# Optimization experiments

Hardware: AMD Instinct MI355X
Metric: run time of the kernel (lower is better)

## Reference

```python
import jax, jax.numpy as jnp
import numpy as np
from functools import partial

VOCAB = 32000
N_LAYER = 2
D_MODEL = 1024
D_INNER = 2048   # expand * d_model
D_STATE = 16
D_CONV = 4
DT_RANK = 64     # ceil(d_model/16)
SEQ_LEN = 2048   # == D_INNER (required by the repo's conv quirk)
BATCH = 1
EPS = 1e-6


def rmsnorm(x, scale):
    return x * jax.lax.rsqrt(jnp.mean(x * x, axis=-1, keepdims=True) + EPS) * scale


def setup_inputs() -> dict:
    key = jax.random.key(0)
    ks = jax.random.split(key, 16)
    s = 0.02
    L = N_LAYER
    inp = {
        "input_ids": jax.random.randint(ks[0], (BATCH, SEQ_LEN), 0, VOCAB, dtype=jnp.int32),
        "embed": jax.random.normal(ks[1], (VOCAB, D_MODEL), jnp.float32) * s,
        "norm_scale": jnp.ones((L, D_MODEL), jnp.float32),
        "in_proj_w": jax.random.normal(ks[2], (L, D_MODEL, 2 * D_INNER), jnp.float32) * s,
        "in_proj_b": jnp.zeros((L, 2 * D_INNER), jnp.float32),
        "conv_w": jax.random.normal(ks[3], (L, D_CONV, 1, SEQ_LEN), jnp.float32) * s,
        "conv_b": jnp.zeros((L, SEQ_LEN), jnp.float32),
        "x_proj_w": jax.random.normal(ks[4], (L, D_MODEL, DT_RANK + 2 * D_STATE), jnp.float32) * s,
        "dt_proj_w": jax.random.normal(ks[5], (L, DT_RANK, D_INNER), jnp.float32) * s,
        "dt_proj_b": jnp.zeros((L, D_INNER), jnp.float32),
        "out_proj_w": jax.random.normal(ks[6], (L, D_INNER, D_MODEL), jnp.float32) * s,
        "out_proj_b": jnp.zeros((L, D_MODEL), jnp.float32),
        "A_log": jnp.tile(jnp.log(jnp.arange(1, D_STATE + 1, dtype=jnp.float32)), (L, D_INNER, 1)),
        "D_param": jnp.ones((L, D_INNER), jnp.float32),
        "norm_f_scale": jnp.ones((D_MODEL,), jnp.float32),
        "lm_head_w": jax.random.normal(ks[7], (D_MODEL, VOCAB), jnp.float32) * s,
    }
    return inp


def selective_scan(u, delta, A, B, C, D):
    # u, delta: (b,l,d)   A: (d,n)   B,C: (b,l,n)   D: (d,)
    deltaA = jnp.exp(jnp.einsum('bld,dn->bldn', delta, A))            # (b,l,d,n)
    deltaB_u = delta[..., None] * B[:, :, None, :] * u[..., None]      # (b,l,d,n)

    def step(x, inps):
        dA, dBu, c = inps            # (b,d,n),(b,d,n),(b,n)
        x = dA * x + dBu
        y = jnp.einsum('bdn,bn->bd', x, c)
        return x, y

    x0 = jnp.zeros((u.shape[0], u.shape[2], A.shape[1]), u.dtype)
    _, ys = jax.lax.scan(step, x0, (jnp.moveaxis(deltaA, 1, 0),
                                    jnp.moveaxis(deltaB_u, 1, 0),
                                    jnp.moveaxis(C, 1, 0)))
    return jnp.moveaxis(ys, 0, 1) + u * D                              # (b,l,d)


def depthwise_conv(x, w, b):
    # Faithful to repo: Conv(features=SEQ_LEN, groups=D_INNER) on (b, d_inner, l).
    # With SEQ_LEN == D_INNER this is a depthwise conv over the d_inner axis.
    # x: (b, d_inner, l) as (N, W, C);  w: (d_conv, 1, SEQ_LEN)
    y = jax.lax.conv_general_dilated(x, w, window_strides=(1,), padding='SAME',
                                     dimension_numbers=('NWC', 'WIO', 'NWC'),
                                     feature_group_count=SEQ_LEN)
    return y + b


def mamba_block(h, norm_scale, in_w, in_b, conv_w, conv_b, x_proj_w,
                dt_w, dt_b, out_w, out_b, A_log, Dp):
    u = rmsnorm(h, norm_scale)
    A = -jnp.exp(A_log)
    x_and_res = u @ in_w + in_b
    x, res = jnp.split(x_and_res, 2, axis=-1)
    xt = jnp.transpose(x, (0, 2, 1))                 # (b, d_inner, l)
    xt = depthwise_conv(xt, conv_w, conv_b)[:, :, :u.shape[1]]
    x = jax.nn.silu(jnp.transpose(xt, (0, 2, 1)))     # (b, l, d_inner)
    x_dbl = u @ x_proj_w
    delta, B, C = jnp.split(x_dbl, [DT_RANK, DT_RANK + D_STATE], axis=-1)
    delta = jax.nn.softplus(delta @ dt_w + dt_b)
    y = selective_scan(x, delta, A, B, C, Dp)
    y = y * jax.nn.silu(res)
    return y @ out_w + out_b + h


def reference(input_ids, embed, norm_scale, in_proj_w, in_proj_b, conv_w, conv_b,
              x_proj_w, dt_proj_w, dt_proj_b, out_proj_w, out_proj_b, A_log,
              D_param, norm_f_scale, lm_head_w):
    h = embed[input_ids]                              # (b,l,d_model)
    for i in range(N_LAYER):
        h = mamba_block(h, norm_scale[i], in_proj_w[i], in_proj_b[i], conv_w[i],
                        conv_b[i], x_proj_w[i], dt_proj_w[i], dt_proj_b[i],
                        out_proj_w[i], out_proj_b[i], A_log[i], D_param[i])
    h = rmsnorm(h, norm_f_scale)
    return h @ lm_head_w                              # (b,l,vocab)
```

## Files before the change

### kernel.cpp

```cpp
#include <hip/hip_runtime.h>
#include <hip/hip_bf16.h>

#define SEQ 2048
#define DM  1024
#define DI  2048
#define DST 16
#define DTR 64
#define NVOC 32000
#define NVOCP 32768
#define NC  64
#define LC  32

typedef __bf16 bf16x8 __attribute__((ext_vector_type(8)));
typedef float  f32x4  __attribute__((ext_vector_type(4)));

__device__ __forceinline__ float siluf(float x) { return x / (1.f + expf(-x)); }
__device__ __forceinline__ float softplusf(float x) {
    return fmaxf(x, 0.f) + log1pf(expf(-fabsf(x)));
}
__device__ __forceinline__ unsigned short f2bf(float f) {
    union { __hip_bfloat16 h; unsigned short u; } c;
    c.h = __float2bfloat16(f);
    return c.u;
}

__global__ void embed_gather(const int* __restrict__ ids, const float* __restrict__ embed,
                             float* __restrict__ h) {
    int l = blockIdx.x;
    int row = ids[l];
    const float4* src = (const float4*)(embed + (size_t)row * DM);
    float4* dst = (float4*)(h + (size_t)l * DM);
    dst[threadIdx.x] = src[threadIdx.x];
}

__global__ void rmsnorm_kernel(const float* __restrict__ x, const float* __restrict__ w,
                               float* __restrict__ o, unsigned short* __restrict__ ob) {
    int l = blockIdx.x;
    int t = threadIdx.x;
    float4 v = ((const float4*)(x + (size_t)l * DM))[t];
    float ss = v.x*v.x + v.y*v.y + v.z*v.z + v.w*v.w;
    #pragma unroll
    for (int m = 32; m; m >>= 1) ss += __shfl_xor(ss, m);
    __shared__ float red[4];
    if ((t & 63) == 0) red[t >> 6] = ss;
    __syncthreads();
    float tot = red[0] + red[1] + red[2] + red[3];
    float sc = rsqrtf(tot * (1.f / DM) + 1e-6f);
    float4 wv = ((const float4*)w)[t];
    float4 ov;
    ov.x = v.x * sc * wv.x;
    ov.y = v.y * sc * wv.y;
    ov.z = v.z * sc * wv.z;
    ov.w = v.w * sc * wv.w;
    if (ob) {
        uint2 pk;
        pk.x = (unsigned)f2bf(ov.x) | ((unsigned)f2bf(ov.y) << 16);
        pk.y = (unsigned)f2bf(ov.z) | ((unsigned)f2bf(ov.w) << 16);
        ((uint2*)(ob + (size_t)l * DM))[t] = pk;
    } else {
        ((float4*)(o + (size_t)l * DM))[t] = ov;
    }
}

__global__ void transpose_all(const float* __restrict__ in_w, const float* __restrict__ xp_w,
                              const float* __restrict__ out_w, const float* __restrict__ dt_w,
                              const float* __restrict__ lm_w,
                              unsigned short* __restrict__ in_wT, unsigned short* __restrict__ out_wT,
                              unsigned short* __restrict__ dt_wT, unsigned short* __restrict__ lm_wT) {
    int b = blockIdx.x;
    const float* W; unsigned short* WT; int K, N, Np, loc;
    if      (b < 1024)  { W = in_w;                        WT = in_wT;                                             K=1024; N=4096;  Np=4096;  loc = b; }
    else if (b < 1056)  { W = xp_w;                        WT = in_wT + (size_t)4096 * 1024;                       K=1024; N=96;    Np=128;   loc = b - 1024; }
    else if (b < 2080)  { W = in_w + (size_t)1024 * 4096;  WT = in_wT + (size_t)4224 * 1024;                       K=1024; N=4096;  Np=4096;  loc = b - 1056; }
    else if (b < 2112)  { W = xp_w + (size_t)1024 * 96;    WT = in_wT + (size_t)4224 * 1024 + (size_t)4096 * 1024; K=1024; N=96;    Np=128;   loc = b - 2080; }
    else if (b < 2624)  { W = out_w;                       WT = out_wT;                                            K=2048; N=1024;  Np=1024;  loc = b - 2112; }
    else if (b < 3136)  { W = out_w + (size_t)2048 * 1024; WT = out_wT + (size_t)1024 * 2048;                      K=2048; N=1024;  Np=1024;  loc = b - 2624; }
    else if (b < 3168)  { W = dt_w;                        WT = dt_wT;                                             K=64;   N=2048;  Np=2048;  loc = b - 3136; }
    else if (b < 3200)  { W = dt_w + (size_t)64 * 2048;    WT = dt_wT + (size_t)2048 * 64;                         K=64;   N=2048;  Np=2048;  loc = b - 3168; }
    else                { if (!lm_wT) return; W = lm_w;    WT = lm_wT;                                             K=1024; N=32000; Np=32768; loc = b - 3200; }
    int tiles_x = Np >> 6;
    int n0 = (loc % tiles_x) * 64, k0 = (loc / tiles_x) * 64;
    __shared__ float tile[64][65];
    int tx = threadIdx.x;
    int ty = threadIdx.y;
    #pragma unroll
    for (int i = 0; i < 8; i++) {
        int r = ty + i * 8;
        int n1 = n0 + tx, n2 = n0 + tx + 32;
        tile[tx][r]      = (n1 < N) ? W[(size_t)(k0 + r) * N + n1] : 0.f;
        tile[tx + 32][r] = (n2 < N) ? W[(size_t)(k0 + r) * N + n2] : 0.f;
    }
    __syncthreads();
    int t = ty * 32 + tx;
    int nrow = t >> 5;
    int u = t & 31;
    #pragma unroll
    for (int pass = 0; pass < 8; pass++) {
        int n = pass * 8 + nrow;
        unsigned v = (unsigned)f2bf(tile[n][2 * u]) | ((unsigned)f2bf(tile[n][2 * u + 1]) << 16);
        *(unsigned*)&WT[(size_t)(n0 + n) * K + k0 + 2 * u] = v;
    }
}

template<int ACT>
__global__ __launch_bounds__(256) void gemm_f32(const float* __restrict__ A, int lda,
                                                const float* __restrict__ B,
                                                const float* __restrict__ bias,
                                                const float* __restrict__ add,
                                                float* __restrict__ C,
                                                int M, int N, int K) {
    __shared__ float As[16][68];
    __shared__ float Bs[16][64];
    int tx = threadIdx.x, ty = threadIdx.y;
    int t = ty * 16 + tx;
    int m0 = blockIdx.y * 64, n0 = blockIdx.x * 64;
    float acc[4][4] = {};
    for (int k0 = 0; k0 < K; k0 += 16) {
        #pragma unroll
        for (int i = 0; i < 4; i++) {
            int idx = t + i * 256;
            int mm = idx >> 4, kk = idx & 15;
            As[kk][mm] = A[(size_t)(m0 + mm) * lda + k0 + kk];
            int nn = idx & 63, k2 = idx >> 6;
            Bs[k2][nn] = B[(size_t)(k0 + k2) * N + n0 + nn];
        }
        __syncthreads();
        #pragma unroll
        for (int kk = 0; kk < 16; kk++) {
            float4 a = *(const float4*)&As[kk][ty * 4];
            float4 b = *(const float4*)&Bs[kk][tx * 4];
            acc[0][0] += a.x*b.x; acc[0][1] += a.x*b.y; acc[0][2] += a.x*b.z; acc[0][3] += a.x*b.w;
            acc[1][0] += a.y*b.x; acc[1][1] += a.y*b.y; acc[1][2] += a.y*b.z; acc[1][3] += a.y*b.w;
            acc[2][0] += a.z*b.x; acc[2][1] += a.z*b.y; acc[2][2] += a.z*b.z; acc[2][3] += a.z*b.w;
            acc[3][0] += a.w*b.x; acc[3][1] += a.w*b.y; acc[3][2] += a.w*b.z; acc[3][3] += a.w*b.w;
        }
        __syncthreads();
    }
    #pragma unroll
    for (int i = 0; i < 4; i++) {
        int row = m0 + ty * 4 + i;
        float4 r;
        float* pr = &r.x;
        #pragma unroll
        for (int j = 0; j < 4; j++) {
            int col = n0 + tx * 4 + j;
            float v = acc[i][j];
            if (bias) v += bias[col];
            if (add)  v += add[(size_t)row * N + col];
            if (ACT == 1) v = softplusf(v);
            pr[j] = v;
        }
        *(float4*)&C[(size_t)row * N + n0 + tx * 4] = r;
    }
}

template<int BIAS, int ADD, int ACT, int XP>
__global__ __launch_bounds__(256) void gemm_bf16(const unsigned short* __restrict__ A, int lda,
                                                 const unsigned short* __restrict__ BT,
                                                 const float* __restrict__ bias,
                                                 const float* __restrict__ add,
                                                 float* __restrict__ C,
                                                 float* __restrict__ xp_out,
                                                 unsigned short* __restrict__ aux,
                                                 int M, int N, int K) {
    __shared__ unsigned short As[128 * 32];
    __shared__ unsigned short Bs[128 * 32];
    int t = threadIdx.x;
    int w = t >> 6, l = t & 63;
    int wm = w >> 1, wn = w & 1;
    int m0 = blockIdx.x * 128;
    int n0 = blockIdx.y * 128;
    int lr = l & 15, lk = (l >> 4) * 8;
    int sr = t >> 2, sc = (t & 3) * 8;
    f32x4 acc[4][4] = {};
    for (int k0 = 0; k0 < K; k0 += 32) {
        const unsigned short* ga = A  + (size_t)(m0 + sr) * lda + k0 + sc;
        const unsigned short* gb = BT + (size_t)(n0 + sr) * K + k0 + sc;
        unsigned short* la = As + w * 512;
        unsigned short* lb = Bs + w * 512;
        __builtin_amdgcn_global_load_lds((const __attribute__((address_space(1))) void*)ga,
            (__attribute__((address_space(3))) void*)la, 16, 0, 0);
        __builtin_amdgcn_global_load_lds((const __attribute__((address_space(1))) void*)(ga + (size_t)64 * lda),
            (__attribute__((address_space(3))) void*)(la + 2048), 16, 0, 0);
        __builtin_amdgcn_global_load_lds((const __attribute__((address_space(1))) void*)gb,
            (__attribute__((address_space(3))) void*)(lb), 16, 0, 0);
        __builtin_amdgcn_global_load_lds((const __attribute__((address_space(1))) void*)(gb + (size_t)64 * K),
            (__attribute__((address_space(3))) void*)(lb + 2048), 16, 0, 0);
        __syncthreads();
        bf16x8 af[4], bfr[4];
        #pragma unroll
        for (int i = 0; i < 4; i++) {
            af[i]  = *reinterpret_cast<const bf16x8*>(&As[(wm * 64 + i * 16 + lr) * 32 + lk]);
            bfr[i] = *reinterpret_cast<const bf16x8*>(&Bs[(wn * 64 + i * 16 + lr) * 32 + lk]);
        }
        #pragma unroll
        for (int i = 0; i < 4; i++)
            #pragma unroll
            for (int j = 0; j < 4; j++)
                acc[i][j] = __builtin_amdgcn_mfma_f32_16x16x32_bf16(af[i], bfr[j], acc[i][j], 0, 0, 0);
        __syncthreads();
    }
    int cr = (l >> 4) * 4;
    if (XP && n0 >= 4096) {
        #pragma unroll
        for (int i = 0; i < 4; i++) {
            #pragma unroll
            for (int j = 0; j < 4; j++) {
                int c2 = (n0 - 4096) + wn * 64 + j * 16 + lr;
                #pragma unroll
                for (int rr = 0; rr < 4; rr++) {
                    int row = m0 + wm * 64 + i * 16 + cr + rr;
                    float v = acc[i][j][rr];
                    xp_out[(size_t)row * 128 + c2] = v;
                    if (c2 < 64) aux[(size_t)row * 64 + c2] = f2bf(v);
                }
            }
        }
    } else {
        int ldc = XP ? 4096 : N;
        #pragma unroll
        for (int i = 0; i < 4; i++) {
            #pragma unroll
            for (int j = 0; j < 4; j++) {
                int col = n0 + wn * 64 + j * 16 + lr;
                float bv = BIAS ? bias[col] : 0.f;
                #pragma unroll
                for (int rr = 0; rr < 4; rr++) {
                    int row = m0 + wm * 64 + i * 16 + cr + rr;
                    float v = acc[i][j][rr] + bv;
                    if (ADD) v += add[(size_t)row * ldc + col];
                    if (ACT == 1) v = softplusf(v);
                    C[(size_t)row * ldc + col] = v;
                }
            }
        }
    }
}

__global__ __launch_bounds__(1024, 4) void gemm_lm(
        const unsigned short* __restrict__ A,
        const unsigned short* __restrict__ BT,
        float* __restrict__ C, int M, int N, int K) {
    extern __shared__ unsigned short lds[];
    const int t = threadIdx.x;
    const int w = t >> 6, l = t & 63;
    const int wr = w >> 2, wc = w & 3;
    int bxx = blockIdx.x, byy = blockIdx.y;
    if (gridDim.x == 8 && (gridDim.y & 7) == 0) {
        int lin = blockIdx.y * 8 + blockIdx.x;
        int xcd = lin & 7, i = lin >> 3;
        bxx = i & 7;
        byy = xcd * (gridDim.y >> 3) + (i >> 3);
    }
    const int m0 = bxx * 256, n0 = byy * 256;
    const int lr = l & 15;
    const int rowA = wr * 64 + lr;
    const int rowB = wc * 64 + lr;
    const int colR = (((l >> 4) ^ (lr & 3)) * 8);
    const int srow = t >> 2;
    const int scol = (((t & 3) ^ (srow & 3)) * 8);
    const int NT = K >> 5;
    f32x4 acc[4][4] = {};
    bf16x8 af[4], bf[4];

    const unsigned short* gA = A  + (size_t)(m0 + srow) * K + scol;
    const unsigned short* gB = BT + (size_t)(n0 + srow) * K + scol;

    #pragma unroll
    for (int pp = 0; pp < 2; pp++) {
        if (pp < NT) {
            unsigned short* Ld = lds + pp * 16384;
            __builtin_amdgcn_global_load_lds(
                (const __attribute__((address_space(1))) void*)(gA + pp * 32),
                (__attribute__((address_space(3))) void*)(Ld + w * 512), 16, 0, 0);
            __builtin_amdgcn_global_load_lds(
                (const __attribute__((address_space(1))) void*)(gB + pp * 32),
                (__attribute__((address_space(3))) void*)(Ld + 8192 + w * 512), 16, 0, 0);
        }
    }

    for (int kt = 0; kt < NT; kt++) {
        if (kt >= NT - 2) { asm volatile("s_waitcnt vmcnt(0)" ::: "memory"); }
        else              { asm volatile("s_waitcnt vmcnt(2)" ::: "memory"); }
        __builtin_amdgcn_sched_barrier(0);
        __builtin_amdgcn_s_barrier();
        __builtin_amdgcn_sched_barrier(0);
        const unsigned short* Ab = lds + (kt % 3) * 16384;
        const unsigned short* Bb = Ab + 8192;
        #pragma unroll
        for (int i = 0; i < 4; i++)
            af[i] = *reinterpret_cast<const bf16x8*>(&Ab[(rowA + i * 16) * 32 + colR]);
        #pragma unroll
        for (int j = 0; j < 4; j++)
            bf[j] = *reinterpret_cast<const bf16x8*>(&Bb[(rowB + j * 16) * 32 + colR]);
        if (kt + 2 < NT) {
            unsigned short* Ld = lds + ((kt + 2) % 3) * 16384;
            __builtin_amdgcn_global_load_lds(
                (const __attribute__((address_space(1))) void*)(gA + (kt + 2) * 32),
                (__attribute__((address_space(3))) void*)(Ld + w * 512), 16, 0, 0);
            __builtin_amdgcn_global_load_lds(
                (const __attribute__((address_space(1))) void*)(gB + (kt + 2) * 32),
                (__attribute__((address_space(3))) void*)(Ld + 8192 + w * 512), 16, 0, 0);
        }
        __builtin_amdgcn_s_setprio(1);
        #pragma unroll
        for (int i = 0; i < 4; i++)
            #pragma unroll
            for (int j = 0; j < 4; j++)
                acc[i][j] = __builtin_amdgcn_mfma_f32_16x16x32_bf16(af[i], bf[j], acc[i][j], 0, 0, 0);
        __builtin_amdgcn_s_setprio(0);
    }

    float* cf = (float*)lds;
    const int cr = (l >> 4) * 4;
    for (int r = 0; r < 4; r++) {
        __syncthreads();
        if (wr == r) {
            #pragma unroll
            for (int i = 0; i < 4; i++)
                #pragma unroll
                for (int j = 0; j < 4; j++) {
                    int col = wc * 64 + j * 16 + lr;
                    #pragma unroll
                    for (int rr = 0; rr < 4; rr++)
                        cf[(i * 16 + cr + rr) * 260 + col] = acc[i][j][rr];
                }
        }
        __syncthreads();
        #pragma unroll
        for (int pass = 0; pass < 4; pass++) {
            int row = pass * 16 + (t >> 6);
            int f4 = t & 63;
            float4 v = *(const float4*)&cf[row * 260 + f4 * 4];
            int grow = m0 + r * 64 + row;
            int gcol = n0 + f4 * 4;
            if (gcol < N) *(float4*)&C[(size_t)grow * N + gcol] = v;
        }
    }
}

__global__ void xproj_kernel(const float* __restrict__ u, const float* __restrict__ xw,
                             float* __restrict__ xdbl) {
    int l0 = blockIdx.x * 4;
    int t = threadIdx.x;
    __shared__ float us[4][DM];
    for (int i = t; i < 4 * DM; i += 128) us[i >> 10][i & 1023] = u[(size_t)l0 * DM + i];
    __syncthreads();
    if (t < 96) {
        float a0 = 0.f, a1 = 0.f, a2 = 0.f, a3 = 0.f;
        for (int k = 0; k < DM; k++) {
            float wv = xw[(size_t)k * 96 + t];
            a0 += us[0][k] * wv; a1 += us[1][k] * wv;
            a2 += us[2][k] * wv; a3 += us[3][k] * wv;
        }
        xdbl[(size_t)(l0 + 0) * 128 + t] = a0;
        xdbl[(size_t)(l0 + 1) * 128 + t] = a1;
        xdbl[(size_t)(l0 + 2) * 128 + t] = a2;
        xdbl[(size_t)(l0 + 3) * 128 + t] = a3;
    }
}

__global__ __launch_bounds__(256) void scan_p1(const float* __restrict__ xr,
        const float* __restrict__ delta, const float* __restrict__ xdbl,
        const float* __restrict__ cw, const float* __restrict__ cb,
        const float* __restrict__ A_log, float* __restrict__ P, float* __restrict__ S) {
    int c = blockIdx.x;
    int d = blockIdx.y * 256 + threadIdx.x;
    int l0 = c * LC;
    __shared__ float Bsh[LC][16];
    __shared__ float cwsh[4][LC];
    __shared__ float cbsh[LC];
    {
        int t = threadIdx.x;
        #pragma unroll
        for (int i = t; i < LC * 16; i += 256) {
            int ll = i >> 4, q = i & 15;
            Bsh[ll][q] = xdbl[(size_t)(l0 + ll) * 128 + 64 + q];
        }
        if (t < LC) {
            cbsh[t] = cb[l0 + t];
            #pragma unroll
            for (int k = 0; k < 4; k++) cwsh[k][t] = cw[k * SEQ + l0 + t];
        }
    }
    __syncthreads();
    float a[16];
    #pragma unroll
    for (int i = 0; i < 4; i++) {
        float4 al = ((const float4*)(A_log + (size_t)d * 16))[i];
        a[4*i+0] = -expf(al.x); a[4*i+1] = -expf(al.y);
        a[4*i+2] = -expf(al.z); a[4*i+3] = -expf(al.w);
    }
    float s[16] = {};
    float sumdv = 0.f;
    for (int ll = 0; ll < LC; ll++) {
        size_t lrow = (size_t)(l0 + ll);
        float dv = delta[lrow * DI + d];
        const float* xrow = xr + lrow * 4096;
        float accv = cbsh[ll];
        #pragma unroll
        for (int k = 0; k < 4; k++) {
            int cc = d + k - 1;
            if (cc >= 0 && cc < DI) accv += xrow[cc] * cwsh[k][ll];
        }
        float xv = siluf(accv);
        float du = dv * xv;
        sumdv += dv;
        #pragma unroll
        for (int n = 0; n < 16; n++)
            s[n] = expf(dv * a[n]) * s[n] + du * Bsh[ll][n];
    }
    size_t o = ((size_t)c * DI + d) * 16;
    #pragma unroll
    for (int i = 0; i < 4; i++) {
        float4 sv = make_float4(s[4*i], s[4*i+1], s[4*i+2], s[4*i+3]);
        float4 pv = make_float4(expf(a[4*i]*sumdv), expf(a[4*i+1]*sumdv),
                                expf(a[4*i+2]*sumdv), expf(a[4*i+3]*sumdv));
        ((float4*)(S + o))[i] = sv;
        ((float4*)(P + o))[i] = pv;
    }
}

__global__ void scan_p2(const float* __restrict__ P, const float* __restrict__ S,
                        float* __restrict__ X) {
    int t = blockIdx.x * 256 + threadIdx.x;
    float x = 0.f;
    #pragma unroll 16
    for (int c = 0; c < NC; c++) {
        X[(size_t)c * (DI*16) + t] = x;
        x = P[(size_t)c * (DI*16) + t] * x + S[(size_t)c * (DI*16) + t];
    }
}

__global__ __launch_bounds__(256) void scan_p3(const float* __restrict__ xr,
        const float* __restrict__ delta, const float* __restrict__ xdbl,
        const float* __restrict__ cw, const float* __restrict__ cb,
        const float* __restrict__ A_log, const float* __restrict__ Dp,
        const float* __restrict__ X,
        float* __restrict__ y, unsigned short* __restrict__ yb) {
    int c = blockIdx.x;
    int d = blockIdx.y * 256 + threadIdx.x;
    int l0 = c * LC;
    __shared__ float Bsh[LC][16], Csh[LC][16];
    __shared__ float cwsh[4][LC];
    __shared__ float cbsh[LC];
    {
        int t = threadIdx.x;
        #pragma unroll
        for (int i = t; i < LC * 16; i += 256) {
            int ll = i >> 4, q = i & 15;
            size_t row = (size_t)(l0 + ll) * 128;
            Bsh[ll][q] = xdbl[row + 64 + q];
            Csh[ll][q] = xdbl[row + 80 + q];
        }
        if (t < LC) {
            cbsh[t] = cb[l0 + t];
            #pragma unroll
            for (int k = 0; k < 4; k++) cwsh[k][t] = cw[k * SEQ + l0 + t];
        }
    }
    __syncthreads();
    float a[16];
    #pragma unroll
    for (int i = 0; i < 4; i++) {
        float4 al = ((const float4*)(A_log + (size_t)d * 16))[i];
        a[4*i+0] = -expf(al.x); a[4*i+1] = -expf(al.y);
        a[4*i+2] = -expf(al.z); a[4*i+3] = -expf(al.w);
    }
    float s[16];
    size_t o = ((size_t)c * DI + d) * 16;
    #pragma unroll
    for (int i = 0; i < 4; i++) {
        float4 xv4 = ((const float4*)(X + o))[i];
        s[4*i] = xv4.x; s[4*i+1] = xv4.y; s[4*i+2] = xv4.z; s[4*i+3] = xv4.w;
    }
    float Dv = Dp[d];
    for (int ll = 0; ll < LC; ll++) {
        size_t lrow = (size_t)(l0 + ll);
        float dv = delta[lrow * DI + d];
        const float* xrow = xr + lrow * 4096;
        float accv = cbsh[ll];
        #pragma unroll
        for (int k = 0; k < 4; k++) {
            int cc = d + k - 1;
            if (cc >= 0 && cc < DI) accv += xrow[cc] * cwsh[k][ll];
        }
        float xv = siluf(accv);
        float du = dv * xv;
        float yv = 0.f;
        #pragma unroll
        for (int n = 0; n < 16; n++) {
            s[n] = expf(dv * a[n]) * s[n] + du * Bsh[ll][n];
            yv += s[n] * Csh[ll][n];
        }
        float res = xrow[2048 + d];
        float val = (yv + xv * Dv) * siluf(res);
        if (yb) yb[lrow * DI + d] = f2bf(val);
        else    y[lrow * DI + d] = val;
    }
}

extern "C" void kernel_launch(void* const* d_in, const int* in_sizes, int n_in,
                              void* d_out, int out_size, void* d_ws, size_t ws_size,
                              hipStream_t stream) {
    const int*   ids        = (const int*)d_in[0];
    const float* embed      = (const float*)d_in[1];
    const float* norm_scale = (const float*)d_in[2];
    const float* in_w       = (const float*)d_in[3];
    const float* in_b       = (const float*)d_in[4];
    const float* conv_w     = (const float*)d_in[5];
    const float* conv_b     = (const float*)d_in[6];
    const float* x_proj_w   = (const float*)d_in[7];
    const float* dt_w       = (const float*)d_in[8];
    const float* dt_b       = (const float*)d_in[9];
    const float* out_w      = (const float*)d_in[10];
    const float* out_b      = (const float*)d_in[11];
    const float* A_log      = (const float*)d_in[12];
    const float* Dp         = (const float*)d_in[13];
    const float* norm_f     = (const float*)d_in[14];
    const float* lm_w       = (const float*)d_in[15];

    float* out = (float*)d_out;

    char* p = (char*)d_ws;
    float* h  = (float*)p;  p += (size_t)SEQ * DM * 4;
    float* hn = (float*)p;  p += (size_t)SEQ * DM * 4;
    size_t base = (size_t)p - (size_t)d_ws;
    const size_t SZ_UB    = (size_t)SEQ * DM * 2;
    const size_t SZ_YB    = (size_t)SEQ * DI * 2;
    const size_t SZ_HNB   = (size_t)SEQ * DM * 2;
    const size_t SZ_DB    = (size_t)SEQ * 64 * 2;
    const size_t SZ_INWT  = (size_t)2 * 4224 * DM * 2;
    const size_t SZ_OUTWT = (size_t)2 * DM * DI * 2;
    const size_t SZ_DTWT  = (size_t)2 * DI * 64 * 2;
    const size_t SZ_LMWT  = (size_t)NVOCP * DM * 2;
    size_t need_mid  = base + SZ_UB + SZ_YB + SZ_HNB + SZ_DB + SZ_INWT + SZ_OUTWT + SZ_DTWT;
    size_t need_full = need_mid + SZ_LMWT;
    bool mid  = ws_size >= need_mid;
    bool full = ws_size >= need_full;

    unsigned short *u_b = nullptr, *y_b = nullptr, *hn_b = nullptr, *dlt_b = nullptr;
    unsigned short *in_wT = nullptr, *out_wT = nullptr, *dt_wT = nullptr, *lm_wT = nullptr;
    if (mid) {
        u_b    = (unsigned short*)p; p += SZ_UB;
        y_b    = (unsigned short*)p; p += SZ_YB;
        hn_b   = (unsigned short*)p; p += SZ_HNB;
        dlt_b  = (unsigned short*)p; p += SZ_DB;
        in_wT  = (unsigned short*)p; p += SZ_INWT;
        out_wT = (unsigned short*)p; p += SZ_OUTWT;
        dt_wT  = (unsigned short*)p; p += SZ_DTWT;
        if (full) { lm_wT = (unsigned short*)p; p += SZ_LMWT; }
    }

    float* u     = out;
    float* xr    = u + (size_t)SEQ * DM;
    float* xdbl  = xr + (size_t)SEQ * 4096;
    float* delta = xdbl + (size_t)SEQ * 128;
    float* y     = delta + (size_t)SEQ * DI;
    float* Pbuf  = y + (size_t)SEQ * DI;
    float* Sbuf  = Pbuf + (size_t)NC * DI * 16;
    float* Xbuf  = Sbuf + (size_t)NC * DI * 16;

    if (mid) {
        int nblocks = full ? 11392 : 3200;
        transpose_all<<<nblocks, dim3(32, 8), 0, stream>>>(
            in_w, x_proj_w, out_w, dt_w, lm_w, in_wT, out_wT, dt_wT, lm_wT);
    }

    embed_gather<<<SEQ, 256, 0, stream>>>(ids, embed, h);

    for (int L = 0; L < 2; L++) {
        rmsnorm_kernel<<<SEQ, 256, 0, stream>>>(h, norm_scale + (size_t)L * DM, u, u_b);
        if (mid) {
            gemm_bf16<1, 0, 0, 1><<<dim3(SEQ / 128, 4224 / 128), 256, 0, stream>>>(
                u_b, DM, in_wT + (size_t)L * 4224 * DM, in_b + (size_t)L * 4096, nullptr, xr,
                xdbl, dlt_b, SEQ, 4224, DM);
            gemm_bf16<1, 0, 1, 0><<<dim3(SEQ / 128, DI / 128), 256, 0, stream>>>(
                dlt_b, 64, dt_wT + (size_t)L * DI * 64, dt_b + (size_t)L * DI, nullptr, delta,
                nullptr, nullptr, SEQ, DI, 64);
        } else {
            gemm_f32<0><<<dim3(4096 / 64, SEQ / 64), dim3(16, 16), 0, stream>>>(
                u, DM, in_w + (size_t)L * DM * 4096, in_b + (size_t)L * 4096, nullptr, xr,
                SEQ, 4096, DM);
            xproj_kernel<<<SEQ / 4, 128, 0, stream>>>(u, x_proj_w + (size_t)L * DM * 96, xdbl);
            gemm_f32<1><<<dim3(DI / 64, SEQ / 64), dim3(16, 16), 0, stream>>>(
                xdbl, 128, dt_w + (size_t)L * DTR * DI, dt_b + (size_t)L * DI, nullptr, delta,
                SEQ, DI, DTR);
        }
        scan_p1<<<dim3(NC, DI / 256), 256, 0, stream>>>(
            xr, delta, xdbl, conv_w + (size_t)L * 4 * SEQ, conv_b + (size_t)L * SEQ,
            A_log + (size_t)L * DI * DST, Pbuf, Sbuf);
        scan_p2<<<DI * 16 / 256, 256, 0, stream>>>(Pbuf, Sbuf, Xbuf);
        scan_p3<<<dim3(NC, DI / 256), 256, 0, stream>>>(
            xr, delta, xdbl, conv_w + (size_t)L * 4 * SEQ, conv_b + (size_t)L * SEQ,
            A_log + (size_t)L * DI * DST, Dp + (size_t)L * DI, Xbuf, y, y_b);
        if (mid) {
            gemm_bf16<1, 1, 0, 0><<<dim3(SEQ / 128, DM / 128), 256, 0, stream>>>(
                y_b, DI, out_wT + (size_t)L * DM * DI, out_b + (size_t)L * DM, h, h,
                nullptr, nullptr, SEQ, DM, DI);
        } else {
            gemm_f32<0><<<dim3(DM / 64, SEQ / 64), dim3(16, 16), 0, stream>>>(
                y, DI, out_w + (size_t)L * DI * DM, out_b + (size_t)L * DM, h, h,
                SEQ, DM, DI);
        }
    }

    rmsnorm_kernel<<<SEQ, 256, 0, stream>>>(h, norm_f, hn, full ? hn_b : nullptr);
    if (full) {
        hipFuncSetAttribute((const void*)gemm_lm,
                            hipFuncAttributeMaxDynamicSharedMemorySize, 98304);
        gemm_lm<<<dim3(SEQ / 256, NVOCP / 256), 1024, 98304, stream>>>(
            hn_b, lm_wT, out, SEQ, NVOC, DM);
    } else {
        gemm_f32<0><<<dim3(NVOC / 64, SEQ / 64), dim3(16, 16), 0, stream>>>(
            hn, DM, lm_w, nullptr, nullptr, out, SEQ, NVOC, DM);
    }
}
```

Measured before the change: 807.2 us.

## Fuse three-phase chunked scan into one cooperative kernel with grid syncs

Replaces the three separate scan launches (chunk-local scan, cross-chunk prefix, chunk re-scan) with a single cooperative kernel that uses grid.sync between phases, keeping shared-memory staging and A coefficients live across phases. This removes two kernel launches and their drain gaps per layer. The grid is 512 blocks of 256 threads, which must all be co-resident for the cooperative launch. During the middle phase only 128 blocks work while the rest wait. The lm_head GEMM output store is also switched to a nontemporal store to avoid polluting the cache with the large logits write.

```diff
diff --git a/kernel.cpp b/kernel.cpp
--- a/kernel.cpp
+++ b/kernel.cpp
@@ -1,5 +1,8 @@
 #include <hip/hip_runtime.h>
 #include <hip/hip_bf16.h>
+#include <hip/hip_cooperative_groups.h>
+
+namespace cg = cooperative_groups;
 
 #define SEQ 2048
 #define DM  1024
@@ -331,10 +334,11 @@
         for (int pass = 0; pass < 4; pass++) {
             int row = pass * 16 + (t >> 6);
             int f4 = t & 63;
-            float4 v = *(const float4*)&cf[row * 260 + f4 * 4];
+            f32x4 v = *(const f32x4*)&cf[row * 260 + f4 * 4];
             int grow = m0 + r * 64 + row;
             int gcol = n0 + f4 * 4;
-            if (gcol < N) *(float4*)&C[(size_t)grow * N + gcol] = v;
+            if (gcol < N)
+                __builtin_nontemporal_store(v, (f32x4*)&C[(size_t)grow * N + gcol]);
         }
     }
 }
@@ -360,84 +364,14 @@
     }
 }
 
-__global__ __launch_bounds__(256) void scan_p1(const float* __restrict__ xr,
-        const float* __restrict__ delta, const float* __restrict__ xdbl,
-        const float* __restrict__ cw, const float* __restrict__ cb,
-        const float* __restrict__ A_log, float* __restrict__ P, float* __restrict__ S) {
-    int c = blockIdx.x;
-    int d = blockIdx.y * 256 + threadIdx.x;
-    int l0 = c * LC;
-    __shared__ float Bsh[LC][16];
-    __shared__ float cwsh[4][LC];
-    __shared__ float cbsh[LC];
-    {
-        int t = threadIdx.x;
-        #pragma unroll
-        for (int i = t; i < LC * 16; i += 256) {
-            int ll = i >> 4, q = i & 15;
-            Bsh[ll][q] = xdbl[(size_t)(l0 + ll) * 128 + 64 + q];
-        }
-        if (t < LC) {
-            cbsh[t] = cb[l0 + t];
-            #pragma unroll
-            for (int k = 0; k < 4; k++) cwsh[k][t] = cw[k * SEQ + l0 + t];
-        }
-    }
-    __syncthreads();
-    float a[16];
-    #pragma unroll
-    for (int i = 0; i < 4; i++) {
-        float4 al = ((const float4*)(A_log + (size_t)d * 16))[i];
-        a[4*i+0] = -expf(al.x); a[4*i+1] = -expf(al.y);
-        a[4*i+2] = -expf(al.z); a[4*i+3] = -expf(al.w);
-    }
-    float s[16] = {};
-    float sumdv = 0.f;
-    for (int ll = 0; ll < LC; ll++) {
-        size_t lrow = (size_t)(l0 + ll);
-        float dv = delta[lrow * DI + d];
-        const float* xrow = xr + lrow * 4096;
-        float accv = cbsh[ll];
-        #pragma unroll
-        for (int k = 0; k < 4; k++) {
-            int cc = d + k - 1;
-            if (cc >= 0 && cc < DI) accv += xrow[cc] * cwsh[k][ll];
-        }
-        float xv = siluf(accv);
-        float du = dv * xv;
-        sumdv += dv;
-        #pragma unroll
-        for (int n = 0; n < 16; n++)
-            s[n] = expf(dv * a[n]) * s[n] + du * Bsh[ll][n];
-    }
-    size_t o = ((size_t)c * DI + d) * 16;
-    #pragma unroll
-    for (int i = 0; i < 4; i++) {
-        float4 sv = make_float4(s[4*i], s[4*i+1], s[4*i+2], s[4*i+3]);
-        float4 pv = make_float4(expf(a[4*i]*sumdv), expf(a[4*i+1]*sumdv),
-                                expf(a[4*i+2]*sumdv), expf(a[4*i+3]*sumdv));
-        ((float4*)(S + o))[i] = sv;
-        ((float4*)(P + o))[i] = pv;
-    }
-}
-
-__global__ void scan_p2(const float* __restrict__ P, const float* __restrict__ S,
-                        float* __restrict__ X) {
-    int t = blockIdx.x * 256 + threadIdx.x;
-    float x = 0.f;
-    #pragma unroll 16
-    for (int c = 0; c < NC; c++) {
-        X[(size_t)c * (DI*16) + t] = x;
-        x = P[(size_t)c * (DI*16) + t] * x + S[(size_t)c * (DI*16) + t];
-    }
-}
-
-__global__ __launch_bounds__(256) void scan_p3(const float* __restrict__ xr,
-        const float* __restrict__ delta, const float* __restrict__ xdbl,
-        const float* __restrict__ cw, const float* __restrict__ cb,
-        const float* __restrict__ A_log, const float* __restrict__ Dp,
-        const float* __restrict__ X,
+__global__ __launch_bounds__(256) void scan_fused(
+        const float* __restrict__ xr, const float* __restrict__ delta,
+        const float* __restrict__ xdbl, const float* __restrict__ cw,
+        const float* __restrict__ cb, const float* __restrict__ A_log,
+        const float* __restrict__ Dp,
+        float* __restrict__ P, float* __restrict__ S, float* __restrict__ X,
         float* __restrict__ y, unsigned short* __restrict__ yb) {
+    cg::grid_group grid = cg::this_grid();
     int c = blockIdx.x;
     int d = blockIdx.y * 256 + threadIdx.x;
     int l0 = c * LC;
@@ -467,36 +401,82 @@
         a[4*i+0] = -expf(al.x); a[4*i+1] = -expf(al.y);
         a[4*i+2] = -expf(al.z); a[4*i+3] = -expf(al.w);
     }
-    float s[16];
+    float Dv = Dp[d];
     size_t o = ((size_t)c * DI + d) * 16;
-    #pragma unroll
-    for (int i = 0; i < 4; i++) {
-        float4 xv4 = ((const float4*)(X + o))[i];
-        s[4*i] = xv4.x; s[4*i+1] = xv4.y; s[4*i+2] = xv4.z; s[4*i+3] = xv4.w;
-    }
-    float Dv = Dp[d];
-    for (int ll = 0; ll < LC; ll++) {
-        size_t lrow = (size_t)(l0 + ll);
-        float dv = delta[lrow * DI + d];
-        const float* xrow = xr + lrow * 4096;
-        float accv = cbsh[ll];
-        #pragma unroll
-        for (int k = 0; k < 4; k++) {
-            int cc = d + k - 1;
-            if (cc >= 0 && cc < DI) accv += xrow[cc] * cwsh[k][ll];
-        }
-        float xv = siluf(accv);
-        float du = dv * xv;
-        float yv = 0.f;
-        #pragma unroll
-        for (int n = 0; n < 16; n++) {
-            s[n] = expf(dv * a[n]) * s[n] + du * Bsh[ll][n];
-            yv += s[n] * Csh[ll][n];
-        }
-        float res = xrow[2048 + d];
-        float val = (yv + xv * Dv) * siluf(res);
-        if (yb) yb[lrow * DI + d] = f2bf(val);
-        else    y[lrow * DI + d] = val;
+
+    {
+        float s[16] = {};
+        float sumdv = 0.f;
+        for (int ll = 0; ll < LC; ll++) {
+            size_t lrow = (size_t)(l0 + ll);
+            float dv = delta[lrow * DI + d];
+            const float* xrow = xr + lrow * 4096;
+            float accv = cbsh[ll];
+            #pragma unroll
+            for (int k = 0; k < 4; k++) {
+                int cc = d + k - 1;
+                if (cc >= 0 && cc < DI) accv += xrow[cc] * cwsh[k][ll];
+            }
+            float xv = siluf(accv);
+            float du = dv * xv;
+            sumdv += dv;
+            #pragma unroll
+            for (int n = 0; n < 16; n++)
+                s[n] = expf(dv * a[n]) * s[n] + du * Bsh[ll][n];
+        }
+        #pragma unroll
+        for (int i = 0; i < 4; i++) {
+            float4 sv = make_float4(s[4*i], s[4*i+1], s[4*i+2], s[4*i+3]);
+            float4 pv = make_float4(expf(a[4*i]*sumdv), expf(a[4*i+1]*sumdv),
+                                    expf(a[4*i+2]*sumdv), expf(a[4*i+3]*sumdv));
+            ((float4*)(S + o))[i] = sv;
+            ((float4*)(P + o))[i] = pv;
+        }
+    }
+    grid.sync();
+    {
+        int lin = blockIdx.y * gridDim.x + blockIdx.x;
+        if (lin < (DI * 16) / 256) {
+            int t2 = lin * 256 + threadIdx.x;
+            float x = 0.f;
+            #pragma unroll 16
+            for (int cc = 0; cc < NC; cc++) {
+                X[(size_t)cc * (DI * 16) + t2] = x;
+                x = P[(size_t)cc * (DI * 16) + t2] * x + S[(size_t)cc * (DI * 16) + t2];
+            }
+        }
+    }
+    grid.sync();
+    {
+        float s[16];
+        #pragma unroll
+        for (int i = 0; i < 4; i++) {
+            float4 xv4 = ((const float4*)(X + o))[i];
+            s[4*i] = xv4.x; s[4*i+1] = xv4.y; s[4*i+2] = xv4.z; s[4*i+3] = xv4.w;
+        }
+        for (int ll = 0; ll < LC; ll++) {
+            size_t lrow = (size_t)(l0 + ll);
+            float dv = delta[lrow * DI + d];
+            const float* xrow = xr + lrow * 4096;
+            float accv = cbsh[ll];
+            #pragma unroll
+            for (int k = 0; k < 4; k++) {
+                int cc = d + k - 1;
+                if (cc >= 0 && cc < DI) accv += xrow[cc] * cwsh[k][ll];
+            }
+            float xv = siluf(accv);
+            float du = dv * xv;
+            float yv = 0.f;
+            #pragma unroll
+            for (int n = 0; n < 16; n++) {
+                s[n] = expf(dv * a[n]) * s[n] + du * Bsh[ll][n];
+                yv += s[n] * Csh[ll][n];
+            }
+            float res = xrow[2048 + d];
+            float val = (yv + xv * Dv) * siluf(res);
+            if (yb) yb[lrow * DI + d] = f2bf(val);
+            else    y[lrow * DI + d] = val;
+        }
     }
 }
 
@@ -587,13 +567,24 @@
                 xdbl, 128, dt_w + (size_t)L * DTR * DI, dt_b + (size_t)L * DI, nullptr, delta,
                 SEQ, DI, DTR);
         }
-        scan_p1<<<dim3(NC, DI / 256), 256, 0, stream>>>(
-            xr, delta, xdbl, conv_w + (size_t)L * 4 * SEQ, conv_b + (size_t)L * SEQ,
-            A_log + (size_t)L * DI * DST, Pbuf, Sbuf);
-        scan_p2<<<DI * 16 / 256, 256, 0, stream>>>(Pbuf, Sbuf, Xbuf);
-        scan_p3<<<dim3(NC, DI / 256), 256, 0, stream>>>(
-            xr, delta, xdbl, conv_w + (size_t)L * 4 * SEQ, conv_b + (size_t)L * SEQ,
-            A_log + (size_t)L * DI * DST, Dp + (size_t)L * DI, Xbuf, y, y_b);
+        {
+            const float* cwp = conv_w + (size_t)L * 4 * SEQ;
+            const float* cbp = conv_b + (size_t)L * SEQ;
+            const float* alp = A_log + (size_t)L * DI * DST;
+            const float* dpp = Dp + (size_t)L * DI;
+            const float* xrp = xr;
+            const float* dlp = delta;
+            const float* xdp = xdbl;
+            float* yp = y;
+            unsigned short* ybp = y_b;
+            float* Pp = Pbuf; float* Sp = Sbuf; float* Xp = Xbuf;
+            void* kargs[] = {(void*)&xrp, (void*)&dlp, (void*)&xdp, (void*)&cwp,
+                             (void*)&cbp, (void*)&alp, (void*)&dpp,
+                             (void*)&Pp, (void*)&Sp, (void*)&Xp,
+                             (void*)&yp, (void*)&ybp};
+            (void)hipLaunchCooperativeKernel((const void*)scan_fused, dim3(NC, DI / 256),
+                                             dim3(256), kargs, 0, stream);
+        }
         if (mid) {
             gemm_bf16<1, 1, 0, 0><<<dim3(SEQ / 128, DM / 128), 256, 0, stream>>>(
                 y_b, DI, out_wT + (size_t)L * DM * DI, out_b + (size_t)L * DM, h, h,
@@ -607,8 +598,8 @@
 
     rmsnorm_kernel<<<SEQ, 256, 0, stream>>>(h, norm_f, hn, full ? hn_b : nullptr);
     if (full) {
-        hipFuncSetAttribute((const void*)gemm_lm,
-                            hipFuncAttributeMaxDynamicSharedMemorySize, 98304);
+        (void)hipFuncSetAttribute((const void*)gemm_lm,
+                                  hipFuncAttributeMaxDynamicSharedMemorySize, 98304);
         gemm_lm<<<dim3(SEQ / 256, NVOCP / 256), 1024, 98304, stream>>>(
             hn_b, lm_wT, out, SEQ, NVOC, DM);
     } else {
```

Result: slower. 1.038 ms (+28.6%).
